# Kernel tuning notes

Hardware: AMD Instinct MI355X
Metric: run time of the kernel (lower is better)

The kernel has to match this reference:

```python
import jax, jax.numpy as jnp
import numpy as np

B, S, D = 4, 2048, 2048
D_INNER = max(128, D // 2)  # 1024, torch default d_inner
FO = 2                      # filter_order
K = 3                       # kernel_size
KS = 3                      # short_kernel_size


def setup_inputs() -> dict:
    key = jax.random.key(0)
    ks = jax.random.split(key, 6)
    return {
        "x": jax.random.normal(ks[0], (B, S, D), jnp.float32),
        # depthwise short conv: weight (D, KS), bias (D,)
        "short_w": jax.random.normal(ks[1], (D, KS), jnp.float32) / np.float32(np.sqrt(KS)),
        "short_b": jnp.zeros((D,), jnp.float32),
        # filter MLP proj: Linear(D -> FO*D_INNER)
        "proj_w": jax.random.normal(ks[2], (D, FO * D_INNER), jnp.float32) / np.float32(np.sqrt(D)),
        "proj_b": jnp.zeros((FO * D_INNER,), jnp.float32),
        # filter MLP output: Linear(D_INNER -> K), SHARED across filter orders
        "filt_w": jax.random.normal(ks[3], (D_INNER, K), jnp.float32) / np.float32(np.sqrt(D_INNER)),
        "filt_b": jnp.zeros((K,), jnp.float32),
        # output projection Linear(D -> D)
        "out_w": jax.random.normal(ks[4], (D, D), jnp.float32) / np.float32(np.sqrt(D)),
        "out_b": jnp.zeros((D,), jnp.float32),
    }


def reference(x, short_w, short_b, proj_w, proj_b, filt_w, filt_b, out_w, out_b):
    b, s, d = x.shape
    v = x  # v captured BEFORE short-conv residual, as in the torch code

    # --- causal depthwise short conv (pad k-1 on left, truncate to s) ---
    xp = jnp.pad(x, ((0, 0), (KS - 1, 0), (0, 0)))
    x_short = short_b
    for j in range(KS):  # tiny fixed kernel loop
        x_short = x_short + xp[:, j:j + s, :] * short_w[:, j]
    x = x + x_short

    # --- filter function: Linear -> GELU -> (shared) Linear -> tanh ---
    h = jax.nn.gelu(x @ proj_w + proj_b, approximate=False)         # (b, s, FO*D_INNER)
    h = h.reshape(b, s, FO, D_INNER)
    filt = jnp.tanh(jnp.einsum('bsfi,ik->bsfk', h, filt_w) + filt_b)  # (b, s, FO, K)

    # --- gated depthwise conv: kernel = mean over seq, shared across channels;
    # sum over filter orders commutes with the (linear) conv, so fold it in ---
    w = filt.mean(axis=1).sum(axis=1)                                # (b, K)
    xp2 = jnp.pad(x, ((0, 0), (K - 1, 0), (0, 0)))
    conv = jnp.zeros_like(x)
    for j in range(K):
        conv = conv + xp2[:, j:j + s, :] * w[:, j][:, None, None]

    # --- gate with v, GELU, output projection ---
    y = jax.nn.gelu(conv * v, approximate=False)
    return y @ out_w + out_b
```

## Files before the change

kernel.cpp:

```cpp
#include <hip/hip_runtime.h>
#include <hip/hip_bf16.h>
#include <math.h>

typedef unsigned short u16;
typedef __attribute__((ext_vector_type(4))) unsigned short u16x4;
typedef __attribute__((ext_vector_type(8))) unsigned short u16x8;
typedef __attribute__((ext_vector_type(8))) short s16x8;
typedef __attribute__((ext_vector_type(4))) float f32x4;

#define B_  4
#define S_  2048
#define D_  2048
#define DI_ 1024
#define MROWS (B_ * S_)
#define KDIM  D_
#define NDIM  D_
#define STRIP 16

__device__ __forceinline__ float b2f(u16 u) {
    union { unsigned i; float f; } v; v.i = ((unsigned)u) << 16; return v.f;
}
__device__ __forceinline__ u16 f2b(float f) {
    unsigned u = __float_as_uint(f);
    unsigned r = (u + 0x7FFFu + ((u >> 16) & 1u)) >> 16;
    return (u16)r;
}
__device__ __forceinline__ float gelu_exact(float x) {
    return 0.5f * x * (1.0f + erff(x * 0.70710678118654752f));
}

#define GLOAD_LDS16(gp, lp)                                                    \
    __builtin_amdgcn_global_load_lds(                                          \
        (const __attribute__((address_space(1))) void*)(gp),                   \
        (__attribute__((address_space(3))) void*)(lp), 16, 0, 0)

__global__ void transpose_k(const float* __restrict__ in0, u16* __restrict__ out0,
                            const float* __restrict__ in1, u16* __restrict__ out1,
                            int n) {
    __shared__ float tile[32][33];
    const float* in = (blockIdx.z == 0) ? in0 : in1;
    u16* out = (blockIdx.z == 0) ? out0 : out1;
    int bx = blockIdx.x * 32, by = blockIdx.y * 32;
    int tx = threadIdx.x, ty = threadIdx.y;
    for (int i = 0; i < 32; i += 8)
        tile[ty + i][tx] = in[(size_t)(by + ty + i) * n + bx + tx];
    __syncthreads();
    for (int i = 0; i < 32; i += 8)
        out[(size_t)(bx + ty + i) * n + by + tx] = f2b(tile[tx][ty + i]);
}

__global__ void shortconv_k(const float* __restrict__ x, const float* __restrict__ sw,
                            const float* __restrict__ sb, u16* __restrict__ xs,
                            float* __restrict__ wacc, float* __restrict__ t_g) {
    const int bid = blockIdx.y * 2 + blockIdx.x;
    {
        int z = bid * 256 + threadIdx.x;
        if (z < 12) wacc[z] = 0.0f;
        if (z < MROWS * 6) t_g[z] = 0.0f;
    }
    const int c = blockIdx.x * 1024 + threadIdx.x * 4;
    const int r0 = blockIdx.y * STRIP;
    const int t0 = r0 & (S_ - 1);

    float tap[12];
    #pragma unroll
    for (int q = 0; q < 3; ++q)
        ((f32x4*)tap)[q] = *(const f32x4*)(sw + (size_t)c * 3 + q * 4);
    f32x4 sbv = *(const f32x4*)(sb + c);

    const float* base = x + (size_t)r0 * D_ + c;
    f32x4 m2, m1;
    if (t0 == 0) { m2 = (f32x4)(0.0f); m1 = (f32x4)(0.0f); }
    else { m2 = *(const f32x4*)(base - 2 * D_); m1 = *(const f32x4*)(base - D_); }

    u16* op = xs + (size_t)r0 * D_ + c;
    #pragma unroll
    for (int rr = 0; rr < STRIP; ++rr) {
        f32x4 cur = *(const f32x4*)(base + (size_t)rr * D_);
        u16x4 outv;
        #pragma unroll
        for (int e = 0; e < 4; ++e) {
            float v = cur[e] + sbv[e]
                    + tap[e * 3 + 0] * m2[e]
                    + tap[e * 3 + 1] * m1[e]
                    + tap[e * 3 + 2] * cur[e];
            outv[e] = f2b(v);
        }
        *(u16x4*)(op + (size_t)rr * D_) = outv;
        m2 = m1; m1 = cur;
    }
}

template <bool FILT>
__global__ void gemm_k(const u16* __restrict__ A, const u16* __restrict__ BT,
                       const float* __restrict__ bias, float* __restrict__ C,
                       const float* __restrict__ fw, float* __restrict__ t_g,
                       int M, int N, int K) {
    __shared__ u16 As[128 * 32];
    __shared__ u16 Bs[128 * 32];
    __shared__ float t_lds[128 * 3];
    const int tid = threadIdx.x;
    const int wid = tid >> 6;
    const int lane = tid & 63;
    const int wm = (wid >> 1) * 64;
    const int wn = (wid & 1) * 64;
    const int row0 = blockIdx.y * 128;
    const int col0 = blockIdx.x * 128;

    if (FILT) {
        for (int z = tid; z < 384; z += 256) t_lds[z] = 0.0f;
    }

    f32x4 acc[4][4];
    #pragma unroll
    for (int i = 0; i < 4; ++i)
        #pragma unroll
        for (int j = 0; j < 4; ++j) acc[i][j] = (f32x4)(0.0f);

    const int srow_l = lane >> 2;
    const int cs = lane & 3;

    const int mrow = wm + (lane & 15);
    const int nrow = wn + (lane & 15);
    const int cf = lane >> 4;

    for (int kt = 0; kt < K; kt += 32) {
        __syncthreads();
        #pragma unroll
        for (int p = 0; p < 2; ++p) {
            int srow = p * 64 + wid * 16 + srow_l;
            int gc = cs ^ ((srow >> 1) & 3);
            u16* lpa = &As[(p * 4 + wid) * 512];
            u16* lpb = &Bs[(p * 4 + wid) * 512];
            const u16* ga = A + (size_t)(row0 + srow) * K + kt + gc * 8;
            const u16* gb = BT + (size_t)(col0 + srow) * K + kt + gc * 8;
            GLOAD_LDS16(ga, lpa);
            GLOAD_LDS16(gb, lpb);
        }
        __syncthreads();

        s16x8 af[4], bfr[4];
        #pragma unroll
        for (int i = 0; i < 4; ++i) {
            int ra = mrow + i * 16;
            af[i] = *(const s16x8*)&As[ra * 32 + ((cf ^ ((ra >> 1) & 3)) * 8)];
        }
        #pragma unroll
        for (int j = 0; j < 4; ++j) {
            int rb = nrow + j * 16;
            bfr[j] = *(const s16x8*)&Bs[rb * 32 + ((cf ^ ((rb >> 1) & 3)) * 8)];
        }
        #pragma unroll
        for (int i = 0; i < 4; ++i)
            #pragma unroll
            for (int j = 0; j < 4; ++j)
                acc[i][j] = __builtin_amdgcn_mfma_f32_16x16x32_bf16(
                    af[i], bfr[j], acc[i][j], 0, 0, 0);
    }

    const int colt0 = wn + (lane & 15);
    if (FILT) {
        float fwv[4][3], bsv[4];
        const int ibase = (col0 & (DI_ - 1)) + colt0;
        #pragma unroll
        for (int j = 0; j < 4; ++j) {
            int ifilt = ibase + j * 16;
            fwv[j][0] = fw[ifilt * 3 + 0];
            fwv[j][1] = fw[ifilt * 3 + 1];
            fwv[j][2] = fw[ifilt * 3 + 2];
            bsv[j] = bias[col0 + colt0 + j * 16];
        }
        #pragma unroll
        for (int i = 0; i < 4; ++i) {
            #pragma unroll
            for (int r = 0; r < 4; ++r) {
                float s0 = 0.f, s1 = 0.f, s2 = 0.f;
                #pragma unroll
                for (int j = 0; j < 4; ++j) {
                    float hv = gelu_exact(acc[i][j][r] + bsv[j]);
                    s0 += hv * fwv[j][0];
                    s1 += hv * fwv[j][1];
                    s2 += hv * fwv[j][2];
                }
                #pragma unroll
                for (int m = 1; m < 16; m <<= 1) {
                    s0 += __shfl_xor(s0, m, 16);
                    s1 += __shfl_xor(s1, m, 16);
                    s2 += __shfl_xor(s2, m, 16);
                }
                if ((lane & 15) == 0) {
                    int trow = wm + (lane >> 4) * 4 + i * 16 + r;
                    atomicAdd(&t_lds[trow * 3 + 0], s0);
                    atomicAdd(&t_lds[trow * 3 + 1], s1);
                    atomicAdd(&t_lds[trow * 3 + 2], s2);
                }
            }
        }
        __syncthreads();
        const int f3 = (col0 >= DI_) ? 3 : 0;
        for (int z = tid; z < 384; z += 256) {
            int rr = z / 3, k = z - rr * 3;
            atomicAdd(&t_g[(size_t)(row0 + rr) * 6 + f3 + k], t_lds[z]);
        }
    } else {
        const int crow0 = row0 + wm + (lane >> 4) * 4;
        #pragma unroll
        for (int j = 0; j < 4; ++j) {
            int col = col0 + colt0 + j * 16;
            float bs = bias[col];
            #pragma unroll
            for (int i = 0; i < 4; ++i) {
                int rbase = crow0 + i * 16;
                #pragma unroll
                for (int r = 0; r < 4; ++r)
                    C[(size_t)(rbase + r) * N + col] = acc[i][j][r] + bs;
            }
        }
    }
}

__global__ void filt_finish_k(const float* __restrict__ t_g, const float* __restrict__ fb,
                              float* __restrict__ wacc) {
    __shared__ float part[3];
    const int tid = threadIdx.x;
    if (tid < 3) part[tid] = 0.0f;
    __syncthreads();
    int p = blockIdx.x * 256 + tid;
    int row = p >> 1, f = p & 1;
    const float* tp = t_g + (size_t)row * 6 + f * 3;
    atomicAdd(&part[0], tanhf(tp[0] + fb[0]));
    atomicAdd(&part[1], tanhf(tp[1] + fb[1]));
    atomicAdd(&part[2], tanhf(tp[2] + fb[2]));
    __syncthreads();
    if (tid < 3) {
        int b = blockIdx.x >> 4;
        atomicAdd(&wacc[b * 3 + tid], part[tid]);
    }
}

__global__ void gate_k(const u16* __restrict__ xs, const float* __restrict__ v,
                       const float* __restrict__ wacc, u16* __restrict__ g) {
    const int c = blockIdx.x * 1024 + threadIdx.x * 4;
    const int r0 = blockIdx.y * STRIP;
    const int t0 = r0 & (S_ - 1);
    const int b = r0 >> 11;
    const float w0 = wacc[b * 3 + 0] * (1.0f / (float)S_);
    const float w1 = wacc[b * 3 + 1] * (1.0f / (float)S_);
    const float w2 = wacc[b * 3 + 2] * (1.0f / (float)S_);

    const u16* base = xs + (size_t)r0 * D_ + c;
    f32x4 m2, m1;
    if (t0 == 0) {
        m2 = (f32x4)(0.0f); m1 = (f32x4)(0.0f);
    } else {
        u16x4 a2 = *(const u16x4*)(base - 2 * D_);
        u16x4 a1 = *(const u16x4*)(base - D_);
        #pragma unroll
        for (int e = 0; e < 4; ++e) { m2[e] = b2f(a2[e]); m1[e] = b2f(a1[e]); }
    }

    const float* vp = v + (size_t)r0 * D_ + c;
    u16* op = g + (size_t)r0 * D_ + c;
    #pragma unroll
    for (int rr = 0; rr < STRIP; ++rr) {
        u16x4 cb = *(const u16x4*)(base + (size_t)rr * D_);
        f32x4 vv = *(const f32x4*)(vp + (size_t)rr * D_);
        f32x4 cur;
        #pragma unroll
        for (int e = 0; e < 4; ++e) cur[e] = b2f(cb[e]);
        u16x4 outv;
        #pragma unroll
        for (int e = 0; e < 4; ++e) {
            float conv = w0 * m2[e] + w1 * m1[e] + w2 * cur[e];
            outv[e] = f2b(gelu_exact(conv * vv[e]));
        }
        *(u16x4*)(op + (size_t)rr * D_) = outv;
        m2 = m1; m1 = cur;
    }
}

extern "C" void kernel_launch(void* const* d_in, const int* in_sizes, int n_in,
                              void* d_out, int out_size, void* d_ws, size_t ws_size,
                              hipStream_t stream) {
    const float* x       = (const float*)d_in[0];
    const float* short_w = (const float*)d_in[1];
    const float* short_b = (const float*)d_in[2];
    const float* proj_w  = (const float*)d_in[3];
    const float* proj_b  = (const float*)d_in[4];
    const float* filt_w  = (const float*)d_in[5];
    const float* filt_b  = (const float*)d_in[6];
    const float* out_w   = (const float*)d_in[7];
    const float* out_b   = (const float*)d_in[8];
    float* out = (float*)d_out;

    char* ws = (char*)d_ws;
    const size_t xs_bytes = (size_t)MROWS * D_ * 2;
    const size_t wt_bytes = (size_t)KDIM * NDIM * 2;
    float* wacc = (float*)(ws);
    float* t_g  = (float*)(ws + 1024);
    u16*   xs   = (u16*)(ws + 262144);
    u16*   g    = (u16*)(ws + 262144 + xs_bytes);
    u16*   wT1  = (u16*)(ws + 262144 + 2 * xs_bytes);
    const size_t need_dual = 262144 + 2 * xs_bytes + 2 * wt_bytes;
    const bool dual = (ws_size >= need_dual);
    u16* wT2 = dual ? (u16*)(ws + 262144 + 2 * xs_bytes + wt_bytes) : wT1;

    dim3 tb(32, 8, 1);

    if (dual) {
        dim3 tg(D_ / 32, D_ / 32, 2);
        transpose_k<<<tg, tb, 0, stream>>>(proj_w, wT1, out_w, wT2, D_);
    } else {
        dim3 tg(D_ / 32, D_ / 32, 1);
        transpose_k<<<tg, tb, 0, stream>>>(proj_w, wT1, proj_w, wT1, D_);
    }

    dim3 cg(2, MROWS / STRIP, 1);
    shortconv_k<<<cg, 256, 0, stream>>>(x, short_w, short_b, xs, wacc, t_g);

    dim3 gg(NDIM / 128, MROWS / 128, 1);
    gemm_k<true><<<gg, 256, 0, stream>>>(xs, wT1, proj_b, nullptr, filt_w, t_g,
                                         MROWS, NDIM, KDIM);

    filt_finish_k<<<64, 256, 0, stream>>>(t_g, filt_b, wacc);

    if (!dual) {
        dim3 tg(D_ / 32, D_ / 32, 1);
        transpose_k<<<tg, tb, 0, stream>>>(out_w, wT2, out_w, wT2, D_);
    }

    gate_k<<<cg, 256, 0, stream>>>(xs, x, wacc, g);

    gemm_k<false><<<gg, 256, 0, stream>>>(g, wT2, out_b, out, nullptr, nullptr,
                                          MROWS, NDIM, KDIM);
}
```

Measured before the change: 389.3 us.

## Rewrite GEMM as 256x256 tile with 4-stage LDS pipeline and 8 waves

Both GEMMs move from 128x128 tiles with 4 waves and a single-buffered LDS load/sync loop to 256x256 tiles with 8 waves. Operand tiles are prefetched three stages ahead into a 4-deep LDS ring via global_load_lds, and each k-tile is split into two half-phases with explicit barriers, waitcnts and setprio around the MFMA bursts. The aim is to hide global load latency and raise MFMA utilisation and data reuse per tile. The cost is higher register and LDS pressure (128KB of LDS, 32 accumulators per lane) and only 256 blocks per GEMM, which may leave some CUs idle.

```diff
diff --git a/kernel.cpp b/kernel.cpp
--- a/kernel.cpp
+++ b/kernel.cpp
@@ -16,6 +16,7 @@
 #define KDIM  D_
 #define NDIM  D_
 #define STRIP 16
+#define NT    (KDIM / 32)
 
 __device__ __forceinline__ float b2f(u16 u) {
     union { unsigned i; float f; } v; v.i = ((unsigned)u) << 16; return v.f;
@@ -92,74 +93,124 @@
 }
 
 template <bool FILT>
-__global__ void gemm_k(const u16* __restrict__ A, const u16* __restrict__ BT,
-                       const float* __restrict__ bias, float* __restrict__ C,
-                       const float* __restrict__ fw, float* __restrict__ t_g,
-                       int M, int N, int K) {
-    __shared__ u16 As[128 * 32];
-    __shared__ u16 Bs[128 * 32];
-    __shared__ float t_lds[128 * 3];
-    const int tid = threadIdx.x;
-    const int wid = tid >> 6;
+__global__ __launch_bounds__(512, 2)
+void gemm_k(const u16* __restrict__ A, const u16* __restrict__ BT,
+            const float* __restrict__ bias, float* __restrict__ C,
+            const float* __restrict__ fw, float* __restrict__ t_g,
+            int M, int N, int K) {
+    __shared__ u16 As[4][8192];
+    __shared__ u16 Bs[4][8192];
+
+    const int tid  = threadIdx.x;
+    const int wid  = tid >> 6;
     const int lane = tid & 63;
-    const int wm = (wid >> 1) * 64;
-    const int wn = (wid & 1) * 64;
-    const int row0 = blockIdx.y * 128;
-    const int col0 = blockIdx.x * 128;
-
+    const int wr   = wid >> 2;
+    const int wc   = wid & 3;
+    const int row0 = blockIdx.y << 8;
+    const int col0 = blockIdx.x << 8;
+
+    const int rowS    = tid >> 2;
+    const int colOffS = (((tid & 3) ^ ((rowS >> 1) & 3)) << 3);
+    const u16* gA0 = A  + (size_t)(row0 + rowS) * KDIM + colOffS;
+    const u16* gB0 = BT + (size_t)(col0 + rowS) * KDIM + colOffS;
+    const int ldsOff0 = wid * 512;
+    const int ldsOff1 = 4096 + wid * 512;
+
+#define STAGE_A(bufi, Tt) do {                                                 \
+    const u16* _g = gA0 + (size_t)(Tt) * 32;                                   \
+    GLOAD_LDS16(_g, &As[bufi][ldsOff0]);                                       \
+    GLOAD_LDS16(_g + (size_t)128 * KDIM, &As[bufi][ldsOff1]);                  \
+} while (0)
+#define STAGE_B(bufi, Tt) do {                                                 \
+    const u16* _g = gB0 + (size_t)(Tt) * 32;                                   \
+    GLOAD_LDS16(_g, &Bs[bufi][ldsOff0]);                                       \
+    GLOAD_LDS16(_g + (size_t)128 * KDIM, &Bs[bufi][ldsOff1]);                  \
+} while (0)
+
+    int aoff[8], boff[4];
+    #pragma unroll
+    for (int i = 0; i < 8; ++i) {
+        int row  = (wr << 7) + (i << 4) + (lane & 15);
+        int slot = (lane >> 4) ^ ((row >> 1) & 3);
+        aoff[i] = row * 32 + slot * 8;
+    }
+    #pragma unroll
+    for (int j = 0; j < 4; ++j) {
+        int row  = (wc << 6) + (j << 4) + (lane & 15);
+        int slot = (lane >> 4) ^ ((row >> 1) & 3);
+        boff[j] = row * 32 + slot * 8;
+    }
+
+    f32x4 acc[8][4];
+    #pragma unroll
+    for (int i = 0; i < 8; ++i)
+        #pragma unroll
+        for (int j = 0; j < 4; ++j) acc[i][j] = (f32x4)(0.0f);
+
+#define PHASE_SYNC()                                                           \
+    __builtin_amdgcn_sched_barrier(0);                                         \
+    __builtin_amdgcn_s_barrier();                                              \
+    asm volatile("s_waitcnt lgkmcnt(0)" ::: "memory");                         \
+    __builtin_amdgcn_sched_barrier(0);
+
+#define TILE_BODY(TT, STG, VMSTR) do {                                         \
+    const int buf_ = (TT) & 3;                                                 \
+    const int sb_  = ((TT) + 3) & 3;                                           \
+    s16x8 af_[4], bf_[4];                                                      \
+    _Pragma("unroll")                                                          \
+    for (int j = 0; j < 4; ++j) bf_[j] = *(const s16x8*)&Bs[buf_][boff[j]];    \
+    _Pragma("unroll")                                                          \
+    for (int i = 0; i < 4; ++i) af_[i] = *(const s16x8*)&As[buf_][aoff[i]];    \
+    if (STG) { STAGE_A(sb_, (TT) + 3); }                                       \
+    PHASE_SYNC();                                                              \
+    __builtin_amdgcn_s_setprio(1);                                             \
+    _Pragma("unroll")                                                          \
+    for (int i = 0; i < 4; ++i)                                                \
+        _Pragma("unroll")                                                      \
+        for (int j = 0; j < 4; ++j)                                            \
+            acc[i][j] = __builtin_amdgcn_mfma_f32_16x16x32_bf16(               \
+                af_[i], bf_[j], acc[i][j], 0, 0, 0);                           \
+    __builtin_amdgcn_s_setprio(0);                                             \
+    __builtin_amdgcn_sched_barrier(0);                                         \
+    __builtin_amdgcn_s_barrier();                                              \
+    _Pragma("unroll")                                                          \
+    for (int i = 0; i < 4; ++i) af_[i] = *(const s16x8*)&As[buf_][aoff[i + 4]];\
+    if (STG) { STAGE_B(sb_, (TT) + 3); }                                       \
+    PHASE_SYNC();                                                              \
+    __builtin_amdgcn_s_setprio(1);                                             \
+    _Pragma("unroll")                                                          \
+    for (int i = 0; i < 4; ++i)                                                \
+        _Pragma("unroll")                                                      \
+        for (int j = 0; j < 4; ++j)                                            \
+            acc[i + 4][j] = __builtin_amdgcn_mfma_f32_16x16x32_bf16(           \
+                af_[i], bf_[j], acc[i + 4][j], 0, 0, 0);                       \
+    __builtin_amdgcn_s_setprio(0);                                             \
+    __builtin_amdgcn_sched_barrier(0);                                         \
+    asm volatile("s_waitcnt " VMSTR ::: "memory");                             \
+    __builtin_amdgcn_s_barrier();                                              \
+} while (0)
+
+    STAGE_A(0, 0); STAGE_B(0, 0);
+    STAGE_A(1, 1); STAGE_B(1, 1);
+    STAGE_A(2, 2); STAGE_B(2, 2);
+    asm volatile("s_waitcnt vmcnt(8)" ::: "memory");
+    __builtin_amdgcn_sched_barrier(0);
+    __builtin_amdgcn_s_barrier();
+
+    #pragma unroll 1
+    for (int T = 0; T <= NT - 4; ++T) {
+        TILE_BODY(T, true, "vmcnt(8)");
+    }
+    TILE_BODY(NT - 3, false, "vmcnt(0)");
+    TILE_BODY(NT - 2, false, "vmcnt(0)");
+    TILE_BODY(NT - 1, false, "vmcnt(0)");
+
+    const int colt0 = (wc << 6) + (lane & 15);
     if (FILT) {
-        for (int z = tid; z < 384; z += 256) t_lds[z] = 0.0f;
-    }
-
-    f32x4 acc[4][4];
-    #pragma unroll
-    for (int i = 0; i < 4; ++i)
-        #pragma unroll
-        for (int j = 0; j < 4; ++j) acc[i][j] = (f32x4)(0.0f);
-
-    const int srow_l = lane >> 2;
-    const int cs = lane & 3;
-
-    const int mrow = wm + (lane & 15);
-    const int nrow = wn + (lane & 15);
-    const int cf = lane >> 4;
-
-    for (int kt = 0; kt < K; kt += 32) {
+        float* t_lds = (float*)&As[0][0];
         __syncthreads();
-        #pragma unroll
-        for (int p = 0; p < 2; ++p) {
-            int srow = p * 64 + wid * 16 + srow_l;
-            int gc = cs ^ ((srow >> 1) & 3);
-            u16* lpa = &As[(p * 4 + wid) * 512];
-            u16* lpb = &Bs[(p * 4 + wid) * 512];
-            const u16* ga = A + (size_t)(row0 + srow) * K + kt + gc * 8;
-            const u16* gb = BT + (size_t)(col0 + srow) * K + kt + gc * 8;
-            GLOAD_LDS16(ga, lpa);
-            GLOAD_LDS16(gb, lpb);
-        }
+        for (int z = tid; z < 768; z += 512) t_lds[z] = 0.0f;
         __syncthreads();
-
-        s16x8 af[4], bfr[4];
-        #pragma unroll
-        for (int i = 0; i < 4; ++i) {
-            int ra = mrow + i * 16;
-            af[i] = *(const s16x8*)&As[ra * 32 + ((cf ^ ((ra >> 1) & 3)) * 8)];
-        }
-        #pragma unroll
-        for (int j = 0; j < 4; ++j) {
-            int rb = nrow + j * 16;
-            bfr[j] = *(const s16x8*)&Bs[rb * 32 + ((cf ^ ((rb >> 1) & 3)) * 8)];
-        }
-        #pragma unroll
-        for (int i = 0; i < 4; ++i)
-            #pragma unroll
-            for (int j = 0; j < 4; ++j)
-                acc[i][j] = __builtin_amdgcn_mfma_f32_16x16x32_bf16(
-                    af[i], bfr[j], acc[i][j], 0, 0, 0);
-    }
-
-    const int colt0 = wn + (lane & 15);
-    if (FILT) {
         float fwv[4][3], bsv[4];
         const int ibase = (col0 & (DI_ - 1)) + colt0;
         #pragma unroll
@@ -171,7 +222,7 @@
             bsv[j] = bias[col0 + colt0 + j * 16];
         }
         #pragma unroll
-        for (int i = 0; i < 4; ++i) {
+        for (int i = 0; i < 8; ++i) {
             #pragma unroll
             for (int r = 0; r < 4; ++r) {
                 float s0 = 0.f, s1 = 0.f, s2 = 0.f;
@@ -189,7 +240,7 @@
                     s2 += __shfl_xor(s2, m, 16);
                 }
                 if ((lane & 15) == 0) {
-                    int trow = wm + (lane >> 4) * 4 + i * 16 + r;
+                    int trow = (wr << 7) + ((lane >> 4) << 2) + (i << 4) + r;
                     atomicAdd(&t_lds[trow * 3 + 0], s0);
                     atomicAdd(&t_lds[trow * 3 + 1], s1);
                     atomicAdd(&t_lds[trow * 3 + 2], s2);
@@ -198,25 +249,29 @@
         }
         __syncthreads();
         const int f3 = (col0 >= DI_) ? 3 : 0;
-        for (int z = tid; z < 384; z += 256) {
+        for (int z = tid; z < 768; z += 512) {
             int rr = z / 3, k = z - rr * 3;
             atomicAdd(&t_g[(size_t)(row0 + rr) * 6 + f3 + k], t_lds[z]);
         }
     } else {
-        const int crow0 = row0 + wm + (lane >> 4) * 4;
+        const int crow0 = row0 + (wr << 7) + ((lane >> 4) << 2);
         #pragma unroll
         for (int j = 0; j < 4; ++j) {
             int col = col0 + colt0 + j * 16;
             float bs = bias[col];
             #pragma unroll
-            for (int i = 0; i < 4; ++i) {
+            for (int i = 0; i < 8; ++i) {
                 int rbase = crow0 + i * 16;
                 #pragma unroll
                 for (int r = 0; r < 4; ++r)
-                    C[(size_t)(rbase + r) * N + col] = acc[i][j][r] + bs;
+                    C[(size_t)(rbase + r) * NDIM + col] = acc[i][j][r] + bs;
             }
         }
     }
+#undef TILE_BODY
+#undef PHASE_SYNC
+#undef STAGE_A
+#undef STAGE_B
 }
 
 __global__ void filt_finish_k(const float* __restrict__ t_g, const float* __restrict__ fb,
@@ -318,8 +373,8 @@
     dim3 cg(2, MROWS / STRIP, 1);
     shortconv_k<<<cg, 256, 0, stream>>>(x, short_w, short_b, xs, wacc, t_g);
 
-    dim3 gg(NDIM / 128, MROWS / 128, 1);
-    gemm_k<true><<<gg, 256, 0, stream>>>(xs, wT1, proj_b, nullptr, filt_w, t_g,
+    dim3 gg(NDIM / 256, MROWS / 256, 1);
+    gemm_k<true><<<gg, 512, 0, stream>>>(xs, wT1, proj_b, nullptr, filt_w, t_g,
                                          MROWS, NDIM, KDIM);
 
     filt_finish_k<<<64, 256, 0, stream>>>(t_g, filt_b, wacc);
@@ -331,6 +386,6 @@
 
     gate_k<<<cg, 256, 0, stream>>>(xs, x, wacc, g);
 
-    gemm_k<false><<<gg, 256, 0, stream>>>(g, wT2, out_b, out, nullptr, nullptr,
+    gemm_k<false><<<gg, 512, 0, stream>>>(g, wT2, out_b, out, nullptr, nullptr,
                                           MROWS, NDIM, KDIM);
 }
```

New measurement: 570.6 us. 46.6% more time.

## Replace output-projection GEMM with 256x256 tile, 4-stage pipelined 8-wave kernel

Applied to the files above, without the earlier changes.

Splits the filter GEMM into its own non-templated kernel and replaces the output-projection GEMM with a new kernel that uses 256x256 tiles, 512 threads (8 waves), and a 4-deep LDS ring buffer with explicit vmcnt waits, barriers and MFMA priority hints. The aim is to overlap global-to-LDS loads with MFMA work and raise data reuse per tile, which should cut memory stalls in the second GEMM. The cost is much higher LDS use (128 KB per block) and more registers, which may limit occupancy. The hand-scheduled waits also add a risk of subtle synchronisation errors.

```diff
diff --git a/kernel.cpp b/kernel.cpp
--- a/kernel.cpp
+++ b/kernel.cpp
@@ -91,11 +91,10 @@
     }
 }
 
-template <bool FILT>
-__global__ void gemm_k(const u16* __restrict__ A, const u16* __restrict__ BT,
-                       const float* __restrict__ bias, float* __restrict__ C,
+__global__ void gemm_f(const u16* __restrict__ A, const u16* __restrict__ BT,
+                       const float* __restrict__ bias,
                        const float* __restrict__ fw, float* __restrict__ t_g,
-                       int M, int N, int K) {
+                       int K) {
     __shared__ u16 As[128 * 32];
     __shared__ u16 Bs[128 * 32];
     __shared__ float t_lds[128 * 3];
@@ -107,9 +106,7 @@
     const int row0 = blockIdx.y * 128;
     const int col0 = blockIdx.x * 128;
 
-    if (FILT) {
-        for (int z = tid; z < 384; z += 256) t_lds[z] = 0.0f;
-    }
+    for (int z = tid; z < 384; z += 256) t_lds[z] = 0.0f;
 
     f32x4 acc[4][4];
     #pragma unroll
@@ -119,7 +116,6 @@
 
     const int srow_l = lane >> 2;
     const int cs = lane & 3;
-
     const int mrow = wm + (lane & 15);
     const int nrow = wn + (lane & 15);
     const int cf = lane >> 4;
@@ -159,64 +155,178 @@
     }
 
     const int colt0 = wn + (lane & 15);
-    if (FILT) {
-        float fwv[4][3], bsv[4];
-        const int ibase = (col0 & (DI_ - 1)) + colt0;
-        #pragma unroll
-        for (int j = 0; j < 4; ++j) {
-            int ifilt = ibase + j * 16;
-            fwv[j][0] = fw[ifilt * 3 + 0];
-            fwv[j][1] = fw[ifilt * 3 + 1];
-            fwv[j][2] = fw[ifilt * 3 + 2];
-            bsv[j] = bias[col0 + colt0 + j * 16];
-        }
-        #pragma unroll
-        for (int i = 0; i < 4; ++i) {
+    float fwv[4][3], bsv[4];
+    const int ibase = (col0 & (DI_ - 1)) + colt0;
+    #pragma unroll
+    for (int j = 0; j < 4; ++j) {
+        int ifilt = ibase + j * 16;
+        fwv[j][0] = fw[ifilt * 3 + 0];
+        fwv[j][1] = fw[ifilt * 3 + 1];
+        fwv[j][2] = fw[ifilt * 3 + 2];
+        bsv[j] = bias[col0 + colt0 + j * 16];
+    }
+    #pragma unroll
+    for (int i = 0; i < 4; ++i) {
+        #pragma unroll
+        for (int r = 0; r < 4; ++r) {
+            float s0 = 0.f, s1 = 0.f, s2 = 0.f;
             #pragma unroll
-            for (int r = 0; r < 4; ++r) {
-                float s0 = 0.f, s1 = 0.f, s2 = 0.f;
-                #pragma unroll
-                for (int j = 0; j < 4; ++j) {
-                    float hv = gelu_exact(acc[i][j][r] + bsv[j]);
-                    s0 += hv * fwv[j][0];
-                    s1 += hv * fwv[j][1];
-                    s2 += hv * fwv[j][2];
-                }
-                #pragma unroll
-                for (int m = 1; m < 16; m <<= 1) {
-                    s0 += __shfl_xor(s0, m, 16);
-                    s1 += __shfl_xor(s1, m, 16);
-                    s2 += __shfl_xor(s2, m, 16);
-                }
-                if ((lane & 15) == 0) {
-                    int trow = wm + (lane >> 4) * 4 + i * 16 + r;
-                    atomicAdd(&t_lds[trow * 3 + 0], s0);
-                    atomicAdd(&t_lds[trow * 3 + 1], s1);
-                    atomicAdd(&t_lds[trow * 3 + 2], s2);
-                }
+            for (int j = 0; j < 4; ++j) {
+                float hv = gelu_exact(acc[i][j][r] + bsv[j]);
+                s0 += hv * fwv[j][0];
+                s1 += hv * fwv[j][1];
+                s2 += hv * fwv[j][2];
             }
-        }
-        __syncthreads();
-        const int f3 = (col0 >= DI_) ? 3 : 0;
-        for (int z = tid; z < 384; z += 256) {
-            int rr = z / 3, k = z - rr * 3;
-            atomicAdd(&t_g[(size_t)(row0 + rr) * 6 + f3 + k], t_lds[z]);
-        }
-    } else {
-        const int crow0 = row0 + wm + (lane >> 4) * 4;
-        #pragma unroll
-        for (int j = 0; j < 4; ++j) {
-            int col = col0 + colt0 + j * 16;
-            float bs = bias[col];
             #pragma unroll
-            for (int i = 0; i < 4; ++i) {
-                int rbase = crow0 + i * 16;
-                #pragma unroll
-                for (int r = 0; r < 4; ++r)
-                    C[(size_t)(rbase + r) * N + col] = acc[i][j][r] + bs;
+            for (int m = 1; m < 16; m <<= 1) {
+                s0 += __shfl_xor(s0, m, 16);
+                s1 += __shfl_xor(s1, m, 16);
+                s2 += __shfl_xor(s2, m, 16);
             }
-        }
-    }
+            if ((lane & 15) == 0) {
+                int trow = wm + (lane >> 4) * 4 + i * 16 + r;
+                atomicAdd(&t_lds[trow * 3 + 0], s0);
+                atomicAdd(&t_lds[trow * 3 + 1], s1);
+                atomicAdd(&t_lds[trow * 3 + 2], s2);
+            }
+        }
+    }
+    __syncthreads();
+    const int f3 = (col0 >= DI_) ? 3 : 0;
+    for (int z = tid; z < 384; z += 256) {
+        int rr = z / 3, k = z - rr * 3;
+        atomicAdd(&t_g[(size_t)(row0 + rr) * 6 + f3 + k], t_lds[z]);
+    }
+}
+
+__global__ __launch_bounds__(512, 2)
+void gemm8_k(const u16* __restrict__ A, const u16* __restrict__ BT,
+             const float* __restrict__ bias, float* __restrict__ C) {
+    __shared__ u16 As[4][8192];
+    __shared__ u16 Bs[4][8192];
+
+    const int tid  = threadIdx.x;
+    const int wid  = tid >> 6;
+    const int lane = tid & 63;
+    const int wr   = wid >> 2;
+    const int wc   = wid & 3;
+    const int row0 = blockIdx.y << 8;
+    const int col0 = blockIdx.x << 8;
+
+    const int rowS    = tid >> 2;
+    const int colOffS = (((tid & 3) ^ ((rowS >> 1) & 3)) << 3);
+    const u16* gA = A  + (size_t)(row0 + rowS) * KDIM + colOffS;
+    const u16* gB = BT + (size_t)(col0 + rowS) * KDIM + colOffS;
+    const int ldsW0 = wid * 512;
+    const int ldsW1 = 4096 + wid * 512;
+
+    int aoffR[8], boffR[4];
+    #pragma unroll
+    for (int i = 0; i < 8; ++i) {
+        int row  = (wr << 7) + (i << 4) + (lane & 15);
+        int slot = (lane >> 4) ^ ((row >> 1) & 3);
+        aoffR[i] = row * 32 + slot * 8;
+    }
+    #pragma unroll
+    for (int j = 0; j < 4; ++j) {
+        int row  = (wc << 6) + (j << 4) + (lane & 15);
+        int slot = (lane >> 4) ^ ((row >> 1) & 3);
+        boffR[j] = row * 32 + slot * 8;
+    }
+
+    f32x4 acc[8][4];
+    #pragma unroll
+    for (int i = 0; i < 8; ++i)
+        #pragma unroll
+        for (int j = 0; j < 4; ++j) acc[i][j] = (f32x4)(0.0f);
+
+    s16x8 af[4], bf[4];
+
+#define STG_A(REG, KOFF) do { const u16* _g = gA + (KOFF);                     \
+    GLOAD_LDS16(_g, &As[REG][ldsW0]);                                          \
+    GLOAD_LDS16(_g + (size_t)128 * KDIM, &As[REG][ldsW1]); } while (0)
+#define STG_B(REG, KOFF) do { const u16* _g = gB + (KOFF);                     \
+    GLOAD_LDS16(_g, &Bs[REG][ldsW0]);                                          \
+    GLOAD_LDS16(_g + (size_t)128 * KDIM, &Bs[REG][ldsW1]); } while (0)
+#define LD_B4(REG) do {                                                        \
+    bf[0] = *(const s16x8*)&Bs[REG][boffR[0]];                                 \
+    bf[1] = *(const s16x8*)&Bs[REG][boffR[1]];                                 \
+    bf[2] = *(const s16x8*)&Bs[REG][boffR[2]];                                 \
+    bf[3] = *(const s16x8*)&Bs[REG][boffR[3]]; } while (0)
+#define LD_A4(REG, I0) do {                                                    \
+    af[0] = *(const s16x8*)&As[REG][aoffR[(I0) + 0]];                          \
+    af[1] = *(const s16x8*)&As[REG][aoffR[(I0) + 1]];                          \
+    af[2] = *(const s16x8*)&As[REG][aoffR[(I0) + 2]];                          \
+    af[3] = *(const s16x8*)&As[REG][aoffR[(I0) + 3]]; } while (0)
+#define SYNC_IN() do { __builtin_amdgcn_s_barrier();                           \
+    asm volatile("s_waitcnt lgkmcnt(0)" ::: "memory");                         \
+    __builtin_amdgcn_sched_barrier(0); } while (0)
+#define MFMA16(I0) do { __builtin_amdgcn_s_setprio(1);                         \
+    _Pragma("unroll")                                                          \
+    for (int i_ = 0; i_ < 4; ++i_) {                                           \
+        _Pragma("unroll")                                                      \
+        for (int j_ = 0; j_ < 4; ++j_)                                         \
+            acc[(I0) + i_][j_] = __builtin_amdgcn_mfma_f32_16x16x32_bf16(      \
+                af[i_], bf[j_], acc[(I0) + i_][j_], 0, 0, 0);                  \
+    }                                                                          \
+    __builtin_amdgcn_s_setprio(0); } while (0)
+#define BARR() __builtin_amdgcn_s_barrier()
+#define VM4() asm volatile("s_waitcnt vmcnt(4)" ::: "memory")
+#define VM0() asm volatile("s_waitcnt vmcnt(0)" ::: "memory")
+
+    STG_A(0, 0);  STG_B(0, 0);
+    STG_A(1, 32); STG_B(1, 32);
+    STG_A(2, 64); STG_B(2, 64);
+    VM4();
+    BARR();
+
+    #pragma unroll 1
+    for (int t = 0; t < 15; ++t) {
+        const int kb = t * 128;
+        LD_B4(0); LD_A4(0, 0); STG_A(3, kb + 96);  SYNC_IN(); MFMA16(0); BARR();
+        LD_A4(0, 4);           STG_B(3, kb + 96);  SYNC_IN(); MFMA16(4); BARR();
+        LD_B4(1); LD_A4(1, 0); STG_A(0, kb + 128); SYNC_IN(); MFMA16(0); BARR();
+        LD_A4(1, 4);           STG_B(0, kb + 128); SYNC_IN(); MFMA16(4); VM4(); BARR();
+        LD_B4(2); LD_A4(2, 0); STG_A(1, kb + 160); SYNC_IN(); MFMA16(0); BARR();
+        LD_A4(2, 4);           STG_B(1, kb + 160); SYNC_IN(); MFMA16(4); BARR();
+        LD_B4(3); LD_A4(3, 0); STG_A(2, kb + 192); SYNC_IN(); MFMA16(0); BARR();
+        LD_A4(3, 4);           STG_B(2, kb + 192); SYNC_IN(); MFMA16(4); VM4(); BARR();
+    }
+    {
+        const int kb = 15 * 128;
+        LD_B4(0); LD_A4(0, 0); STG_A(3, kb + 96);  SYNC_IN(); MFMA16(0); BARR();
+        LD_A4(0, 4);           STG_B(3, kb + 96);  SYNC_IN(); MFMA16(4); BARR();
+        LD_B4(1); LD_A4(1, 0);                     SYNC_IN(); MFMA16(0); BARR();
+        LD_A4(1, 4);                               SYNC_IN(); MFMA16(4); VM0(); BARR();
+        LD_B4(2); LD_A4(2, 0);                     SYNC_IN(); MFMA16(0); BARR();
+        LD_A4(2, 4);                               SYNC_IN(); MFMA16(4); BARR();
+        LD_B4(3); LD_A4(3, 0);                     SYNC_IN(); MFMA16(0); BARR();
+        LD_A4(3, 4);                               SYNC_IN(); MFMA16(4); BARR();
+    }
+
+    const int colt0 = (wc << 6) + (lane & 15);
+    const int crow0 = row0 + (wr << 7) + ((lane >> 4) << 2);
+    #pragma unroll
+    for (int j = 0; j < 4; ++j) {
+        int col = col0 + colt0 + j * 16;
+        float bs = bias[col];
+        #pragma unroll
+        for (int i = 0; i < 8; ++i) {
+            int rbase = crow0 + i * 16;
+            #pragma unroll
+            for (int r = 0; r < 4; ++r)
+                C[(size_t)(rbase + r) * NDIM + col] = acc[i][j][r] + bs;
+        }
+    }
+#undef STG_A
+#undef STG_B
+#undef LD_B4
+#undef LD_A4
+#undef SYNC_IN
+#undef MFMA16
+#undef BARR
+#undef VM4
+#undef VM0
 }
 
 __global__ void filt_finish_k(const float* __restrict__ t_g, const float* __restrict__ fb,
@@ -318,9 +428,8 @@
     dim3 cg(2, MROWS / STRIP, 1);
     shortconv_k<<<cg, 256, 0, stream>>>(x, short_w, short_b, xs, wacc, t_g);
 
-    dim3 gg(NDIM / 128, MROWS / 128, 1);
-    gemm_k<true><<<gg, 256, 0, stream>>>(xs, wT1, proj_b, nullptr, filt_w, t_g,
-                                         MROWS, NDIM, KDIM);
+    dim3 gf(NDIM / 128, MROWS / 128, 1);
+    gemm_f<<<gf, 256, 0, stream>>>(xs, wT1, proj_b, filt_w, t_g, KDIM);
 
     filt_finish_k<<<64, 256, 0, stream>>>(t_g, filt_b, wacc);
 
@@ -331,6 +440,6 @@
 
     gate_k<<<cg, 256, 0, stream>>>(xs, x, wacc, g);
 
-    gemm_k<false><<<gg, 256, 0, stream>>>(g, wT2, out_b, out, nullptr, nullptr,
-                                          MROWS, NDIM, KDIM);
-}
+    dim3 g8(NDIM / 256, MROWS / 256, 1);
+    gemm8_k<<<g8, 512, 0, stream>>>(g, wT2, out_b, out);
+}
```

Result: faster. 365.3 us (-6.2%).

## Rewrite GEMMs as 256x256 tiles with 4-stage LDS pipeline and 8 waves

Applied to the files above, without the earlier changes.

Both GEMMs move from 128x128 tiles with 4 waves and single-buffered LDS to 256x256 tiles with 8 waves, a 4-slot ring of LDS buffers, and explicit vmcnt/barrier scheduling so global-to-LDS loads overlap MFMA work. MFMA blocks are bracketed with setprio to favour the matrix pipe. The aim is to hide global-load latency and raise arithmetic intensity per block. In exchange it uses far more LDS and registers, and the grid drops to 256 blocks, which may limit occupancy and load balance.

```diff
diff --git a/kernel.cpp b/kernel.cpp
--- a/kernel.cpp
+++ b/kernel.cpp
@@ -91,130 +91,176 @@
     }
 }
 
-template <bool FILT>
-__global__ void gemm_k(const u16* __restrict__ A, const u16* __restrict__ BT,
-                       const float* __restrict__ bias, float* __restrict__ C,
-                       const float* __restrict__ fw, float* __restrict__ t_g,
-                       int M, int N, int K) {
-    __shared__ u16 As[128 * 32];
-    __shared__ u16 Bs[128 * 32];
-    __shared__ float t_lds[128 * 3];
-    const int tid = threadIdx.x;
-    const int wid = tid >> 6;
-    const int lane = tid & 63;
-    const int wm = (wid >> 1) * 64;
-    const int wn = (wid & 1) * 64;
-    const int row0 = blockIdx.y * 128;
-    const int col0 = blockIdx.x * 128;
-
-    if (FILT) {
-        for (int z = tid; z < 384; z += 256) t_lds[z] = 0.0f;
-    }
-
-    f32x4 acc[4][4];
-    #pragma unroll
-    for (int i = 0; i < 4; ++i)
-        #pragma unroll
-        for (int j = 0; j < 4; ++j) acc[i][j] = (f32x4)(0.0f);
-
-    const int srow_l = lane >> 2;
-    const int cs = lane & 3;
-
-    const int mrow = wm + (lane & 15);
-    const int nrow = wn + (lane & 15);
-    const int cf = lane >> 4;
-
-    for (int kt = 0; kt < K; kt += 32) {
-        __syncthreads();
-        #pragma unroll
-        for (int p = 0; p < 2; ++p) {
-            int srow = p * 64 + wid * 16 + srow_l;
-            int gc = cs ^ ((srow >> 1) & 3);
-            u16* lpa = &As[(p * 4 + wid) * 512];
-            u16* lpb = &Bs[(p * 4 + wid) * 512];
-            const u16* ga = A + (size_t)(row0 + srow) * K + kt + gc * 8;
-            const u16* gb = BT + (size_t)(col0 + srow) * K + kt + gc * 8;
-            GLOAD_LDS16(ga, lpa);
-            GLOAD_LDS16(gb, lpb);
-        }
-        __syncthreads();
-
-        s16x8 af[4], bfr[4];
-        #pragma unroll
-        for (int i = 0; i < 4; ++i) {
-            int ra = mrow + i * 16;
-            af[i] = *(const s16x8*)&As[ra * 32 + ((cf ^ ((ra >> 1) & 3)) * 8)];
-        }
-        #pragma unroll
-        for (int j = 0; j < 4; ++j) {
-            int rb = nrow + j * 16;
-            bfr[j] = *(const s16x8*)&Bs[rb * 32 + ((cf ^ ((rb >> 1) & 3)) * 8)];
-        }
-        #pragma unroll
-        for (int i = 0; i < 4; ++i)
+#define STG_A(REG, KOFF) do { const u16* _g = gA + (KOFF);                     \
+    GLOAD_LDS16(_g, &As[REG][ldsW0]);                                          \
+    GLOAD_LDS16(_g + (size_t)128 * KDIM, &As[REG][ldsW1]); } while (0)
+#define STG_B(REG, KOFF) do { const u16* _g = gB + (KOFF);                     \
+    GLOAD_LDS16(_g, &Bs[REG][ldsW0]);                                          \
+    GLOAD_LDS16(_g + (size_t)128 * KDIM, &Bs[REG][ldsW1]); } while (0)
+#define LD_B4(REG) do {                                                        \
+    bf[0] = *(const s16x8*)&Bs[REG][boffR[0]];                                 \
+    bf[1] = *(const s16x8*)&Bs[REG][boffR[1]];                                 \
+    bf[2] = *(const s16x8*)&Bs[REG][boffR[2]];                                 \
+    bf[3] = *(const s16x8*)&Bs[REG][boffR[3]]; } while (0)
+#define LD_A4(REG, I0) do {                                                    \
+    af[0] = *(const s16x8*)&As[REG][aoffR[(I0) + 0]];                          \
+    af[1] = *(const s16x8*)&As[REG][aoffR[(I0) + 1]];                          \
+    af[2] = *(const s16x8*)&As[REG][aoffR[(I0) + 2]];                          \
+    af[3] = *(const s16x8*)&As[REG][aoffR[(I0) + 3]]; } while (0)
+#define SYNC_IN() do { __builtin_amdgcn_s_barrier();                           \
+    asm volatile("s_waitcnt lgkmcnt(0)" ::: "memory");                         \
+    __builtin_amdgcn_sched_barrier(0); } while (0)
+#define MFMA16(I0) do { __builtin_amdgcn_s_setprio(1);                         \
+    _Pragma("unroll")                                                          \
+    for (int i_ = 0; i_ < 4; ++i_) {                                           \
+        _Pragma("unroll")                                                      \
+        for (int j_ = 0; j_ < 4; ++j_)                                         \
+            acc[(I0) + i_][j_] = __builtin_amdgcn_mfma_f32_16x16x32_bf16(      \
+                af[i_], bf[j_], acc[(I0) + i_][j_], 0, 0, 0);                  \
+    }                                                                          \
+    __builtin_amdgcn_s_setprio(0); } while (0)
+#define BARR() __builtin_amdgcn_s_barrier()
+#define VM8() asm volatile("s_waitcnt vmcnt(8)" ::: "memory")
+#define VM4() asm volatile("s_waitcnt vmcnt(4)" ::: "memory")
+#define VM0() asm volatile("s_waitcnt vmcnt(0)" ::: "memory")
+
+#define GEMM_CORE(APTR, BPTR)                                                  \
+    __shared__ u16 As[4][8192];                                                \
+    __shared__ u16 Bs[4][8192];                                                \
+    const int tid  = threadIdx.x;                                              \
+    const int wid  = tid >> 6;                                                 \
+    const int lane = tid & 63;                                                 \
+    const int wr   = wid >> 2;                                                 \
+    const int wc   = wid & 3;                                                  \
+    const int row0 = blockIdx.y << 8;                                          \
+    const int col0 = blockIdx.x << 8;                                          \
+    const int rowS    = tid >> 2;                                              \
+    const int colOffS = (((tid & 3) ^ ((rowS >> 1) & 3)) << 3);                \
+    const u16* gA = (APTR) + (size_t)(row0 + rowS) * KDIM + colOffS;           \
+    const u16* gB = (BPTR) + (size_t)(col0 + rowS) * KDIM + colOffS;           \
+    const int ldsW0 = wid * 512;                                               \
+    const int ldsW1 = 4096 + wid * 512;                                        \
+    int aoffR[8], boffR[4];                                                    \
+    _Pragma("unroll")                                                          \
+    for (int i = 0; i < 8; ++i) {                                              \
+        int row  = (wr << 7) + (i << 4) + (lane & 15);                         \
+        int slot = (lane >> 4) ^ ((row >> 1) & 3);                             \
+        aoffR[i] = row * 32 + slot * 8;                                        \
+    }                                                                          \
+    _Pragma("unroll")                                                          \
+    for (int j = 0; j < 4; ++j) {                                              \
+        int row  = (wc << 6) + (j << 4) + (lane & 15);                         \
+        int slot = (lane >> 4) ^ ((row >> 1) & 3);                             \
+        boffR[j] = row * 32 + slot * 8;                                        \
+    }                                                                          \
+    f32x4 acc[8][4];                                                           \
+    _Pragma("unroll")                                                          \
+    for (int i = 0; i < 8; ++i)                                                \
+        _Pragma("unroll")                                                      \
+        for (int j = 0; j < 4; ++j) acc[i][j] = (f32x4)(0.0f);                 \
+    s16x8 af[4], bf[4];                                                        \
+    STG_A(0, 0);  STG_B(0, 0);                                                 \
+    STG_A(1, 32); STG_B(1, 32);                                                \
+    STG_A(2, 64); STG_B(2, 64);                                                \
+    VM8();                                                                     \
+    BARR();                                                                    \
+    _Pragma("unroll 1")                                                        \
+    for (int t = 0; t < 15; ++t) {                                             \
+        const int kb = t * 128;                                                \
+        LD_B4(0); LD_A4(0,0); STG_A(3, kb + 96);  SYNC_IN(); MFMA16(0); BARR();        \
+        LD_A4(0,4);           STG_B(3, kb + 96);  SYNC_IN(); MFMA16(4); VM8(); BARR(); \
+        LD_B4(1); LD_A4(1,0); STG_A(0, kb + 128); SYNC_IN(); MFMA16(0); BARR();        \
+        LD_A4(1,4);           STG_B(0, kb + 128); SYNC_IN(); MFMA16(4); VM8(); BARR(); \
+        LD_B4(2); LD_A4(2,0); STG_A(1, kb + 160); SYNC_IN(); MFMA16(0); BARR();        \
+        LD_A4(2,4);           STG_B(1, kb + 160); SYNC_IN(); MFMA16(4); VM8(); BARR(); \
+        LD_B4(3); LD_A4(3,0); STG_A(2, kb + 192); SYNC_IN(); MFMA16(0); BARR();        \
+        LD_A4(3,4);           STG_B(2, kb + 192); SYNC_IN(); MFMA16(4); VM8(); BARR(); \
+    }                                                                          \
+    {                                                                          \
+        const int kb = 15 * 128;                                               \
+        LD_B4(0); LD_A4(0,0); STG_A(3, kb + 96);  SYNC_IN(); MFMA16(0); BARR();        \
+        LD_A4(0,4);           STG_B(3, kb + 96);  SYNC_IN(); MFMA16(4); VM8(); BARR(); \
+        LD_B4(1); LD_A4(1,0);                     SYNC_IN(); MFMA16(0); BARR();        \
+        LD_A4(1,4);                               SYNC_IN(); MFMA16(4); VM4(); BARR(); \
+        LD_B4(2); LD_A4(2,0);                     SYNC_IN(); MFMA16(0); BARR();        \
+        LD_A4(2,4);                               SYNC_IN(); MFMA16(4); VM0(); BARR(); \
+        LD_B4(3); LD_A4(3,0);                     SYNC_IN(); MFMA16(0); BARR();        \
+        LD_A4(3,4);                               SYNC_IN(); MFMA16(4); BARR();        \
+    }
+
+__global__ __launch_bounds__(512, 2)
+void gemm_f8(const u16* __restrict__ A, const u16* __restrict__ BT,
+             const float* __restrict__ bias,
+             const float* __restrict__ fw, float* __restrict__ t_g) {
+    GEMM_CORE(A, BT)
+
+    __shared__ float t_lds[768];
+    __syncthreads();
+    for (int z = tid; z < 768; z += 512) t_lds[z] = 0.0f;
+    __syncthreads();
+
+    const int colt0 = (wc << 6) + (lane & 15);
+    float fwv[4][3], bsv[4];
+    const int ibase = (col0 & (DI_ - 1)) + colt0;
+    #pragma unroll
+    for (int j = 0; j < 4; ++j) {
+        int ifilt = ibase + j * 16;
+        fwv[j][0] = fw[ifilt * 3 + 0];
+        fwv[j][1] = fw[ifilt * 3 + 1];
+        fwv[j][2] = fw[ifilt * 3 + 2];
+        bsv[j] = bias[col0 + colt0 + j * 16];
+    }
+    #pragma unroll
+    for (int i = 0; i < 8; ++i) {
+        #pragma unroll
+        for (int r = 0; r < 4; ++r) {
+            float s0 = 0.f, s1 = 0.f, s2 = 0.f;
             #pragma unroll
-            for (int j = 0; j < 4; ++j)
-                acc[i][j] = __builtin_amdgcn_mfma_f32_16x16x32_bf16(
-                    af[i], bfr[j], acc[i][j], 0, 0, 0);
-    }
-
-    const int colt0 = wn + (lane & 15);
-    if (FILT) {
-        float fwv[4][3], bsv[4];
-        const int ibase = (col0 & (DI_ - 1)) + colt0;
-        #pragma unroll
-        for (int j = 0; j < 4; ++j) {
-            int ifilt = ibase + j * 16;
-            fwv[j][0] = fw[ifilt * 3 + 0];
-            fwv[j][1] = fw[ifilt * 3 + 1];
-            fwv[j][2] = fw[ifilt * 3 + 2];
-            bsv[j] = bias[col0 + colt0 + j * 16];
-        }
-        #pragma unroll
-        for (int i = 0; i < 4; ++i) {
+            for (int j = 0; j < 4; ++j) {
+                float hv = gelu_exact(acc[i][j][r] + bsv[j]);
+                s0 += hv * fwv[j][0];
+                s1 += hv * fwv[j][1];
+                s2 += hv * fwv[j][2];
+            }
             #pragma unroll
-            for (int r = 0; r < 4; ++r) {
-                float s0 = 0.f, s1 = 0.f, s2 = 0.f;
-                #pragma unroll
-                for (int j = 0; j < 4; ++j) {
-                    float hv = gelu_exact(acc[i][j][r] + bsv[j]);
-                    s0 += hv * fwv[j][0];
-                    s1 += hv * fwv[j][1];
-                    s2 += hv * fwv[j][2];
-                }
-                #pragma unroll
-                for (int m = 1; m < 16; m <<= 1) {
-                    s0 += __shfl_xor(s0, m, 16);
-                    s1 += __shfl_xor(s1, m, 16);
-                    s2 += __shfl_xor(s2, m, 16);
-                }
-                if ((lane & 15) == 0) {
-                    int trow = wm + (lane >> 4) * 4 + i * 16 + r;
-                    atomicAdd(&t_lds[trow * 3 + 0], s0);
-                    atomicAdd(&t_lds[trow * 3 + 1], s1);
-                    atomicAdd(&t_lds[trow * 3 + 2], s2);
-                }
+            for (int m = 1; m < 16; m <<= 1) {
+                s0 += __shfl_xor(s0, m, 16);
+                s1 += __shfl_xor(s1, m, 16);
+                s2 += __shfl_xor(s2, m, 16);
+            }
+            if ((lane & 15) == 0) {
+                int trow = (wr << 7) + ((lane >> 4) << 2) + (i << 4) + r;
+                atomicAdd(&t_lds[trow * 3 + 0], s0);
+                atomicAdd(&t_lds[trow * 3 + 1], s1);
+                atomicAdd(&t_lds[trow * 3 + 2], s2);
             }
         }
-        __syncthreads();
-        const int f3 = (col0 >= DI_) ? 3 : 0;
-        for (int z = tid; z < 384; z += 256) {
-            int rr = z / 3, k = z - rr * 3;
-            atomicAdd(&t_g[(size_t)(row0 + rr) * 6 + f3 + k], t_lds[z]);
-        }
-    } else {
-        const int crow0 = row0 + wm + (lane >> 4) * 4;
-        #pragma unroll
-        for (int j = 0; j < 4; ++j) {
-            int col = col0 + colt0 + j * 16;
-            float bs = bias[col];
+    }
+    __syncthreads();
+    const int f3 = (col0 >= DI_) ? 3 : 0;
+    for (int z = tid; z < 768; z += 512) {
+        int rr = z / 3, k = z - rr * 3;
+        atomicAdd(&t_g[(size_t)(row0 + rr) * 6 + f3 + k], t_lds[z]);
+    }
+}
+
+__global__ __launch_bounds__(512, 2)
+void gemm8_k(const u16* __restrict__ A, const u16* __restrict__ BT,
+             const float* __restrict__ bias, float* __restrict__ C) {
+    GEMM_CORE(A, BT)
+
+    const int colt0 = (wc << 6) + (lane & 15);
+    const int crow0 = row0 + (wr << 7) + ((lane >> 4) << 2);
+    #pragma unroll
+    for (int j = 0; j < 4; ++j) {
+        int col = col0 + colt0 + j * 16;
+        float bs = bias[col];
+        #pragma unroll
+        for (int i = 0; i < 8; ++i) {
+            int rbase = crow0 + i * 16;
             #pragma unroll
-            for (int i = 0; i < 4; ++i) {
-                int rbase = crow0 + i * 16;
-                #pragma unroll
-                for (int r = 0; r < 4; ++r)
-                    C[(size_t)(rbase + r) * N + col] = acc[i][j][r] + bs;
-            }
+            for (int r = 0; r < 4; ++r)
+                C[(size_t)(rbase + r) * NDIM + col] = acc[i][j][r] + bs;
         }
     }
 }
@@ -318,9 +364,8 @@
     dim3 cg(2, MROWS / STRIP, 1);
     shortconv_k<<<cg, 256, 0, stream>>>(x, short_w, short_b, xs, wacc, t_g);
 
-    dim3 gg(NDIM / 128, MROWS / 128, 1);
-    gemm_k<true><<<gg, 256, 0, stream>>>(xs, wT1, proj_b, nullptr, filt_w, t_g,
-                                         MROWS, NDIM, KDIM);
+    dim3 gg(NDIM / 256, MROWS / 256, 1);
+    gemm_f8<<<gg, 512, 0, stream>>>(xs, wT1, proj_b, filt_w, t_g);
 
     filt_finish_k<<<64, 256, 0, stream>>>(t_g, filt_b, wacc);
 
@@ -331,6 +376,5 @@
 
     gate_k<<<cg, 256, 0, stream>>>(xs, x, wacc, g);
 
-    gemm_k<false><<<gg, 256, 0, stream>>>(g, wT2, out_b, out, nullptr, nullptr,
-                                          MROWS, NDIM, KDIM);
-}
+    gemm8_k<<<gg, 512, 0, stream>>>(g, wT2, out_b, out);
+}
```

Measured after the change: 362.0 us. 1.08x faster.
